# Performance work log

Hardware: AMD Instinct MI355X
Metric: run time of the kernel (lower is better)

## Reference

```python
import jax, jax.numpy as jnp
import numpy as np

B, C, N, H = 4, 256, 4096, 4
DK = C // H


def _proj(x, w, b):
    # Conv1d with kernel size 1 == per-point linear: [B,C,N] x [O,C] -> [B,O,N]
    return jnp.einsum('oc,bcn->bon', w, x) + b[None, :, None]


def setup_inputs() -> dict:
    key = jax.random.key(0)
    ks = jax.random.split(key, 9)
    s = 1.0 / np.sqrt(C)
    return {
        'x': jax.random.normal(ks[0], (B, C, N), jnp.float32),
        'wq': jax.random.normal(ks[1], (C, C), jnp.float32) * s,
        'bq': jax.random.normal(ks[2], (C,), jnp.float32) * 0.01,
        'wk': jax.random.normal(ks[3], (C, C), jnp.float32) * s,
        'bk': jax.random.normal(ks[4], (C,), jnp.float32) * 0.01,
        'wv': jax.random.normal(ks[5], (C, C), jnp.float32) * s,
        'bv': jax.random.normal(ks[6], (C,), jnp.float32) * 0.01,
        'wp': jax.random.normal(ks[7], (C, C), jnp.float32) * s,
        'bp': jax.random.normal(ks[8], (C,), jnp.float32) * 0.01,
    }


def reference(x, wq, bq, wk, bk, wv, bv, wp, bp):
    b, c, n = x.shape
    q = _proj(x, wq, bq).reshape(b, H, DK, n)
    k = _proj(x, wk, bk).reshape(b, H, DK, n)
    v = _proj(x, wv, bv).reshape(b, H, DK, n)
    scale = 1.0 / jnp.sqrt(jnp.asarray(DK, x.dtype))
    # scores over point pairs: [B,H,N,N]
    scores = jnp.einsum('bhdn,bhdm->bhnm', q, k) * scale
    attn = jax.nn.softmax(scores, axis=-1)
    out = jnp.einsum('bhnm,bhdm->bhdn', attn, v)  # [B,H,DK,N]
    out = out.reshape(b, c, n)
    out = _proj(out, wp, bp)
    return out + x
```

## Files before the change

### kernel.cpp

```cpp
#include <hip/hip_runtime.h>


#define BDIM 4
#define CDIM 256
#define NDIM 4096
#define HDIM 4
#define DKDIM 64
#define NQ   (BDIM * HDIM * NDIM)
#define QSCALE 0.18033688011112042f

typedef __bf16 bf16x8 __attribute__((ext_vector_type(8)));
typedef float f32x4 __attribute__((ext_vector_type(4)));
typedef short s16x4 __attribute__((ext_vector_type(4)));
typedef unsigned short u16;

__device__ __forceinline__ u16 f2bf(float f) {
  union { __bf16 h; u16 s; } u; u.h = (__bf16)f; return u.s;
}
__device__ __forceinline__ float bf2f(u16 v) {
  union { unsigned u; float f; } x; x.u = (unsigned)v << 16; return x.f;
}

__global__ __launch_bounds__(256) void wcvt_kernel(
    const float* __restrict__ w0, const float* __restrict__ w1,
    const float* __restrict__ w2, const float* __restrict__ w3,
    u16* __restrict__ d0, u16* __restrict__ d1,
    u16* __restrict__ d2, u16* __restrict__ d3)
{
  const int row = blockIdx.x;
  const int m = blockIdx.y;
  const float* s = (m == 0) ? w0 : (m == 1) ? w1 : (m == 2) ? w2 : w3;
  u16* d = (m == 0) ? d0 : (m == 1) ? d1 : (m == 2) ? d2 : d3;
  const float sc = (m == 0) ? QSCALE : 1.0f;
  const int idx = row * CDIM + threadIdx.x;
  d[idx] = f2bf(s[idx] * sc);
}

__global__ __launch_bounds__(256) void xt_kernel(
    const float* __restrict__ x, u16* __restrict__ xT)
{
  const int b = blockIdx.z, c0 = blockIdx.y * 64, n0 = blockIdx.x * 64;
  __shared__ __align__(16) float T[64][68];
  const int t = threadIdx.x;
  {
    const int cr = t >> 4, nc = (t & 15) * 4;
    #pragma unroll
    for (int ci = 0; ci < 4; ++ci) {
      const float4 v = *(const float4*)&x[((size_t)(b * CDIM + c0 + cr + ci * 16)) * NDIM + n0 + nc];
      *(float4*)&T[cr + ci * 16][nc] = v;
    }
  }
  __syncthreads();
  {
    const int n = t >> 2, g = t & 3;
    union { u16 u[16]; uint4 v[2]; } pk;
    #pragma unroll
    for (int u_ = 0; u_ < 16; ++u_) pk.u[u_] = f2bf(T[g * 16 + u_][n]);
    uint4* dst = (uint4*)&xT[((size_t)(b * NDIM + n0 + n)) * CDIM + c0 + g * 16];
    dst[0] = pk.v[0]; dst[1] = pk.v[1];
  }
}

template<int MODE>
__global__ __launch_bounds__(256, 4) void proj_kernel(
    const u16* __restrict__ xT, const u16* __restrict__ wb,
    const float* __restrict__ bias, const float* __restrict__ res,
    void* __restrict__ outp, float bscale)
{
  const int b = blockIdx.z, o0 = blockIdx.y * 64, n0 = blockIdx.x * 64;
  __shared__ __align__(16) u16 XTs[64][40];
  __shared__ __align__(16) u16 Ws[64][40];
  const int t = threadIdx.x, lane = t & 63, w = t >> 6;
  const int qd = lane >> 4, lm = lane & 15;
  const int sr = t >> 2, sg = (t & 3) * 8;

  const u16* xsrc = xT + ((size_t)(b * NDIM + n0 + sr)) * CDIM + sg;
  const u16* wsrc = wb + ((size_t)(o0 + sr)) * CDIM + sg;

  f32x4 acc[4];
  #pragma unroll
  for (int nt = 0; nt < 4; ++nt) acc[nt] = (f32x4){0.f, 0.f, 0.f, 0.f};

  for (int cs = 0; cs < 8; ++cs) {
    __syncthreads();
    *(uint4*)&XTs[sr][sg] = *(const uint4*)(xsrc + cs * 32);
    *(uint4*)&Ws[sr][sg]  = *(const uint4*)(wsrc + cs * 32);
    __syncthreads();
    bf16x8 xf[4];
    #pragma unroll
    for (int nt = 0; nt < 4; ++nt) xf[nt] = *(const bf16x8*)&XTs[16 * nt + lm][qd * 8];
    const bf16x8 wf = *(const bf16x8*)&Ws[16 * w + lm][qd * 8];
    #pragma unroll
    for (int nt = 0; nt < 4; ++nt) {
      if constexpr (MODE == 0)
        acc[nt] = __builtin_amdgcn_mfma_f32_16x16x32_bf16(xf[nt], wf, acc[nt], 0, 0, 0);
      else
        acc[nt] = __builtin_amdgcn_mfma_f32_16x16x32_bf16(wf, xf[nt], acc[nt], 0, 0, 0);
    }
  }

  if constexpr (MODE == 0) {
    u16* out = (u16*)outp;
    const int og = o0 + 16 * w + lm;
    const float bv = bias[og] * bscale;
    #pragma unroll
    for (int nt = 0; nt < 4; ++nt)
      #pragma unroll
      for (int r = 0; r < 4; ++r) {
        const int n = n0 + 16 * nt + 4 * qd + r;
        out[((size_t)(b * NDIM + n)) * CDIM + og] = f2bf(acc[nt][r] + bv);
      }
  } else {
    const float4 b4 = *(const float4*)&bias[o0 + 16 * w + 4 * qd];
    const float bvr[4] = {b4.x, b4.y, b4.z, b4.w};
    #pragma unroll
    for (int nt = 0; nt < 4; ++nt)
      #pragma unroll
      for (int r = 0; r < 4; ++r) {
        const int og = o0 + 16 * w + 4 * qd + r;
        const int n = n0 + 16 * nt + lm;
        const size_t idx = ((size_t)(b * CDIM + og)) * NDIM + n;
        const float val = acc[nt][r] + bvr[r];
        if constexpr (MODE == 1) ((u16*)outp)[idx] = f2bf(val);
        else ((float*)outp)[idx] = val + res[idx];
      }
  }
}

__global__ __launch_bounds__(256, 4) void attn_kernel(
    const u16* __restrict__ qT, const u16* __restrict__ kT,
    const u16* __restrict__ vB, u16* __restrict__ Opart,
    float* __restrict__ Mp, float* __restrict__ Lp)
{
  const int bh = blockIdx.y, b = bh >> 2, h = bh & 3;
  const int n0 = blockIdx.x * 128;
  const int z  = blockIdx.z;
  __shared__ __align__(16) u16 Qt[128][72];
  __shared__ __align__(16) u16 Kt[64][72];
  __shared__ __align__(16) u16 Vt[64][72];

  const int t = threadIdx.x, lane = t & 63, w = t >> 6;
  const int qd = lane >> 4, lm = lane & 15;

  {
    const int r = t >> 1, g = (t & 1) * 32;
    const uint4* src = (const uint4*)&qT[((size_t)(b * NDIM + n0 + r)) * CDIM + h * 64 + g];
    uint4* dst = (uint4*)&Qt[r][g];
    dst[0] = src[0]; dst[1] = src[1]; dst[2] = src[2]; dst[3] = src[3];
  }
  __syncthreads();
  bf16x8 qf[2][2];
  #pragma unroll
  for (int s = 0; s < 2; ++s)
    #pragma unroll
    for (int hh = 0; hh < 2; ++hh)
      qf[s][hh] = *(const bf16x8*)&Qt[16 * (2 * w + s) + lm][32 * hh + qd * 8];

  float m_i[2] = {-1e30f, -1e30f}, l_i[2] = {0.f, 0.f};
  f32x4 oa[2][4];
  #pragma unroll
  for (int s = 0; s < 2; ++s)
    #pragma unroll
    for (int dt = 0; dt < 4; ++dt) oa[s][dt] = (f32x4){0.f, 0.f, 0.f, 0.f};

  const int sr = t >> 2, sg = (t & 3) * 16;
  const u16* kptr = kT + ((size_t)(b * NDIM) + z * 2048 + sr) * CDIM + h * 64 + sg;
  const u16* vptr = vB + ((size_t)(b * CDIM) + h * 64 + sr) * NDIM + z * 2048 + sg;

  for (int it = 0; it < 32; ++it) {
    __syncthreads();
    {
      uint4* kd = (uint4*)&Kt[sr][sg];
      kd[0] = *(const uint4*)(kptr);
      kd[1] = *(const uint4*)(kptr + 8);
      uint4* vd = (uint4*)&Vt[sr][sg];
      vd[0] = *(const uint4*)(vptr);
      vd[1] = *(const uint4*)(vptr + 8);
    }
    kptr += (size_t)64 * CDIM;
    vptr += 64;
    __syncthreads();

    bf16x8 kf[4][2];
    #pragma unroll
    for (int nt = 0; nt < 4; ++nt)
      #pragma unroll
      for (int hh = 0; hh < 2; ++hh)
        kf[nt][hh] = *(const bf16x8*)&Kt[16 * nt + lm][32 * hh + qd * 8];

    float pr[2][4][4];
    #pragma unroll
    for (int s = 0; s < 2; ++s) {
      f32x4 sc[4];
      #pragma unroll
      for (int nt = 0; nt < 4; ++nt) {
        f32x4 zz = (f32x4){0.f, 0.f, 0.f, 0.f};
        zz = __builtin_amdgcn_mfma_f32_16x16x32_bf16(kf[nt][0], qf[s][0], zz, 0, 0, 0);
        zz = __builtin_amdgcn_mfma_f32_16x16x32_bf16(kf[nt][1], qf[s][1], zz, 0, 0, 0);
        sc[nt] = zz;
      }
      float mx = sc[0][0];
      #pragma unroll
      for (int nt = 0; nt < 4; ++nt)
        #pragma unroll
        for (int r = 0; r < 4; ++r) mx = fmaxf(mx, sc[nt][r]);
      mx = fmaxf(mx, __shfl_xor(mx, 16));
      mx = fmaxf(mx, __shfl_xor(mx, 32));
      const float mn = fmaxf(m_i[s], mx);
      if (__any(mx > m_i[s])) {
        const float al = __builtin_amdgcn_exp2f(m_i[s] - mn);
        l_i[s] *= al;
        #pragma unroll
        for (int dt = 0; dt < 4; ++dt) oa[s][dt] *= al;
      }
      m_i[s] = mn;
      float rs = 0.f;
      #pragma unroll
      for (int nt = 0; nt < 4; ++nt)
        #pragma unroll
        for (int r = 0; r < 4; ++r) {
          const float p = __builtin_amdgcn_exp2f(sc[nt][r] - mn);
          pr[s][nt][r] = p;
          rs += p;
        }
      rs += __shfl_xor(rs, 16);
      rs += __shfl_xor(rs, 32);
      l_i[s] += rs;
    }

    #pragma unroll
    for (int c = 0; c < 4; ++c) {
      s16x4 av[4];
      #pragma unroll
      for (int dt = 0; dt < 4; ++dt)
        av[dt] = *(const s16x4*)&Vt[16 * dt + lm][16 * c + 4 * qd];
      union { u16 u[4]; s16x4 v; } bp0, bp1;
      #pragma unroll
      for (int r = 0; r < 4; ++r) { bp0.u[r] = f2bf(pr[0][c][r]); bp1.u[r] = f2bf(pr[1][c][r]); }
      #pragma unroll
      for (int dt = 0; dt < 4; ++dt) {
        oa[0][dt] = __builtin_amdgcn_mfma_f32_16x16x16bf16_1k(av[dt], bp0.v, oa[0][dt], 0, 0, 0);
        oa[1][dt] = __builtin_amdgcn_mfma_f32_16x16x16bf16_1k(av[dt], bp1.v, oa[1][dt], 0, 0, 0);
      }
    }
  }

  __syncthreads();
  u16 (*Ot)[72] = (u16(*)[72])&Qt[0][0];
  #pragma unroll
  for (int s = 0; s < 2; ++s) {
    const float inv = 1.0f / l_i[s];
    #pragma unroll
    for (int dt = 0; dt < 4; ++dt)
      #pragma unroll
      for (int r = 0; r < 4; ++r)
        Ot[16 * (2 * w + s) + lm][16 * dt + 4 * qd + r] = f2bf(oa[s][dt][r] * inv);
  }
  if (qd == 0) {
    const size_t mlbase = ((size_t)z * (BDIM * HDIM) + bh) * NDIM;
    #pragma unroll
    for (int s = 0; s < 2; ++s) {
      const int q = n0 + 16 * (2 * w + s) + lm;
      Mp[mlbase + q] = m_i[s];
      Lp[mlbase + q] = l_i[s];
    }
  }
  __syncthreads();
  {
    const int r = t >> 1, g = (t & 1) * 32;
    u16* dst = Opart + (((size_t)z * (BDIM * HDIM) + bh) * NDIM + n0 + r) * DKDIM + g;
    const uint4* srcp = (const uint4*)&Ot[r][g];
    uint4* d4 = (uint4*)dst;
    d4[0] = srcp[0]; d4[1] = srcp[1]; d4[2] = srcp[2]; d4[3] = srcp[3];
  }
}

__global__ __launch_bounds__(256) void combine_kernel(
    const u16* __restrict__ Opart, const float* __restrict__ Mp,
    const float* __restrict__ Lp, u16* __restrict__ abT)
{
  const int t = threadIdx.x;
  const int gq = blockIdx.x * 64 + (t >> 2);
  const int seg = (t & 3) * 16;
  const float m0 = Mp[gq], l0 = Lp[gq];
  const float m1 = Mp[NQ + gq], l1 = Lp[NQ + gq];
  const float M = fmaxf(m0, m1);
  const float d0 = l0 * __builtin_amdgcn_exp2f(m0 - M);
  const float d1 = l1 * __builtin_amdgcn_exp2f(m1 - M);
  const float inv = 1.0f / (d0 + d1);
  const float w0 = d0 * inv, w1 = d1 * inv;

  const u16* p0 = Opart + (size_t)gq * DKDIM + seg;
  const u16* p1 = Opart + (size_t)NQ * DKDIM + (size_t)gq * DKDIM + seg;
  union { u16 u[16]; uint4 v[2]; } a0, a1, ov;
  a0.v[0] = ((const uint4*)p0)[0]; a0.v[1] = ((const uint4*)p0)[1];
  a1.v[0] = ((const uint4*)p1)[0]; a1.v[1] = ((const uint4*)p1)[1];
  #pragma unroll
  for (int j = 0; j < 16; ++j)
    ov.u[j] = f2bf(w0 * bf2f(a0.u[j]) + w1 * bf2f(a1.u[j]));

  const int bh = gq >> 12, n = gq & (NDIM - 1);
  const int b = bh >> 2, h = bh & 3;
  uint4* dst = (uint4*)&abT[((size_t)(b * NDIM + n)) * CDIM + h * 64 + seg];
  dst[0] = ov.v[0]; dst[1] = ov.v[1];
}

extern "C" void kernel_launch(void* const* d_in, const int* in_sizes, int n_in,
                              void* d_out, int out_size, void* d_ws, size_t ws_size,
                              hipStream_t stream)
{
  const float* x  = (const float*)d_in[0];
  const float* wq = (const float*)d_in[1];
  const float* bq = (const float*)d_in[2];
  const float* wk = (const float*)d_in[3];
  const float* bk = (const float*)d_in[4];
  const float* wv = (const float*)d_in[5];
  const float* bv = (const float*)d_in[6];
  const float* wp = (const float*)d_in[7];
  const float* bp = (const float*)d_in[8];
  float* out = (float*)d_out;

  const size_t sz  = (size_t)BDIM * CDIM * NDIM;
  const size_t wsz = (size_t)CDIM * CDIM;
  u16* xTb = (u16*)d_ws;
  u16* wqb = xTb + sz;
  u16* wkb = wqb + wsz;
  u16* wvb = wkb + wsz;
  u16* wpb = wvb + wsz;
  u16* qTb = wpb + wsz;
  u16* kTb = qTb + sz;
  u16* vBb = kTb + sz;
  u16* abT = vBb + sz;
  u16* Opart = abT + sz;
  float* Mp = (float*)(Opart + 2 * sz);
  float* Lp = Mp + 2 * (size_t)NQ;

  const dim3 blk(256);
  wcvt_kernel<<<dim3(CDIM, 4), blk, 0, stream>>>(wq, wk, wv, wp, wqb, wkb, wvb, wpb);
  xt_kernel<<<dim3(NDIM / 64, CDIM / 64, BDIM), blk, 0, stream>>>(x, xTb);
  const dim3 gp(NDIM / 64, 4, BDIM);
  proj_kernel<0><<<gp, blk, 0, stream>>>(xTb, wqb, bq, nullptr, qTb, QSCALE);
  proj_kernel<0><<<gp, blk, 0, stream>>>(xTb, wkb, bk, nullptr, kTb, 1.0f);
  proj_kernel<1><<<gp, blk, 0, stream>>>(xTb, wvb, bv, nullptr, vBb, 1.0f);
  attn_kernel<<<dim3(NDIM / 128, BDIM * HDIM, 2), blk, 0, stream>>>(qTb, kTb, vBb, Opart, Mp, Lp);
  combine_kernel<<<dim3(NQ / 64), blk, 0, stream>>>(Opart, Mp, Lp, abT);
  proj_kernel<2><<<gp, blk, 0, stream>>>(abT, wpb, bp, x, out, 1.0f);
}
```

Baseline: 232.0 us.

## Fuse weight conversion, QKV projections, and split-K combine into fewer kernels

Drops the separate weight-conversion kernel and converts fp32 weights to bf16 inside the projection tiles. The three Q/K/V projection launches become one launch with a grid dimension selecting the projection. The combine kernel is folded into the output projection, which merges the two attention partials on the fly while staging its input tile. This cuts launches and the abT round trip through memory, at the cost of redoing weight conversion in every tile and making the projection-select branch runtime rather than compile-time.

```diff
diff --git a/kernel.cpp b/kernel.cpp
--- a/kernel.cpp
+++ b/kernel.cpp
@@ -13,27 +13,16 @@
 typedef float f32x4 __attribute__((ext_vector_type(4)));
 typedef short s16x4 __attribute__((ext_vector_type(4)));
 typedef unsigned short u16;
+typedef unsigned int u32;
 
 __device__ __forceinline__ u16 f2bf(float f) {
   union { __bf16 h; u16 s; } u; u.h = (__bf16)f; return u.s;
 }
 __device__ __forceinline__ float bf2f(u16 v) {
-  union { unsigned u; float f; } x; x.u = (unsigned)v << 16; return x.f;
-}
-
-__global__ __launch_bounds__(256) void wcvt_kernel(
-    const float* __restrict__ w0, const float* __restrict__ w1,
-    const float* __restrict__ w2, const float* __restrict__ w3,
-    u16* __restrict__ d0, u16* __restrict__ d1,
-    u16* __restrict__ d2, u16* __restrict__ d3)
-{
-  const int row = blockIdx.x;
-  const int m = blockIdx.y;
-  const float* s = (m == 0) ? w0 : (m == 1) ? w1 : (m == 2) ? w2 : w3;
-  u16* d = (m == 0) ? d0 : (m == 1) ? d1 : (m == 2) ? d2 : d3;
-  const float sc = (m == 0) ? QSCALE : 1.0f;
-  const int idx = row * CDIM + threadIdx.x;
-  d[idx] = f2bf(s[idx] * sc);
+  union { u32 u; float f; } x; x.u = (u32)v << 16; return x.f;
+}
+__device__ __forceinline__ u32 pk2(float a, float b) {
+  return (u32)f2bf(a) | ((u32)f2bf(b) << 16);
 }
 
 __global__ __launch_bounds__(256) void xt_kernel(
@@ -61,13 +50,21 @@
   }
 }
 
-template<int MODE>
-__global__ __launch_bounds__(256, 4) void proj_kernel(
-    const u16* __restrict__ xT, const u16* __restrict__ wb,
-    const float* __restrict__ bias, const float* __restrict__ res,
-    void* __restrict__ outp, float bscale)
-{
-  const int b = blockIdx.z, o0 = blockIdx.y * 64, n0 = blockIdx.x * 64;
+__global__ __launch_bounds__(256, 4) void qkv_kernel(
+    const u16* __restrict__ xT,
+    const float* __restrict__ wq, const float* __restrict__ bq,
+    const float* __restrict__ wk, const float* __restrict__ bk,
+    const float* __restrict__ wv, const float* __restrict__ bv,
+    u16* __restrict__ qT, u16* __restrict__ kT, u16* __restrict__ vB)
+{
+  const int b = blockIdx.z;
+  const int p = blockIdx.y >> 2;
+  const int o0 = (blockIdx.y & 3) * 64;
+  const int n0 = blockIdx.x * 64;
+  const float* wsel = (p == 0) ? wq : (p == 1) ? wk : wv;
+  const float* bsel = (p == 0) ? bq : (p == 1) ? bk : bv;
+  const float wscale = (p == 0) ? QSCALE : 1.0f;
+
   __shared__ __align__(16) u16 XTs[64][40];
   __shared__ __align__(16) u16 Ws[64][40];
   const int t = threadIdx.x, lane = t & 63, w = t >> 6;
@@ -75,7 +72,7 @@
   const int sr = t >> 2, sg = (t & 3) * 8;
 
   const u16* xsrc = xT + ((size_t)(b * NDIM + n0 + sr)) * CDIM + sg;
-  const u16* wsrc = wb + ((size_t)(o0 + sr)) * CDIM + sg;
+  const float* wsrc = wsel + (size_t)(o0 + sr) * CDIM + sg;
 
   f32x4 acc[4];
   #pragma unroll
@@ -84,7 +81,16 @@
   for (int cs = 0; cs < 8; ++cs) {
     __syncthreads();
     *(uint4*)&XTs[sr][sg] = *(const uint4*)(xsrc + cs * 32);
-    *(uint4*)&Ws[sr][sg]  = *(const uint4*)(wsrc + cs * 32);
+    {
+      const float4 w0 = *(const float4*)(wsrc + cs * 32);
+      const float4 w1 = *(const float4*)(wsrc + cs * 32 + 4);
+      union { u32 p[4]; uint4 v; } pw;
+      pw.p[0] = pk2(w0.x * wscale, w0.y * wscale);
+      pw.p[1] = pk2(w0.z * wscale, w0.w * wscale);
+      pw.p[2] = pk2(w1.x * wscale, w1.y * wscale);
+      pw.p[3] = pk2(w1.z * wscale, w1.w * wscale);
+      *(uint4*)&Ws[sr][sg] = pw.v;
+    }
     __syncthreads();
     bf16x8 xf[4];
     #pragma unroll
@@ -92,26 +98,26 @@
     const bf16x8 wf = *(const bf16x8*)&Ws[16 * w + lm][qd * 8];
     #pragma unroll
     for (int nt = 0; nt < 4; ++nt) {
-      if constexpr (MODE == 0)
+      if (p < 2)
         acc[nt] = __builtin_amdgcn_mfma_f32_16x16x32_bf16(xf[nt], wf, acc[nt], 0, 0, 0);
       else
         acc[nt] = __builtin_amdgcn_mfma_f32_16x16x32_bf16(wf, xf[nt], acc[nt], 0, 0, 0);
     }
   }
 
-  if constexpr (MODE == 0) {
-    u16* out = (u16*)outp;
+  if (p < 2) {
+    u16* out = (p == 0) ? qT : kT;
     const int og = o0 + 16 * w + lm;
-    const float bv = bias[og] * bscale;
+    const float bv2 = bsel[og] * wscale;
     #pragma unroll
     for (int nt = 0; nt < 4; ++nt)
       #pragma unroll
       for (int r = 0; r < 4; ++r) {
         const int n = n0 + 16 * nt + 4 * qd + r;
-        out[((size_t)(b * NDIM + n)) * CDIM + og] = f2bf(acc[nt][r] + bv);
+        out[((size_t)(b * NDIM + n)) * CDIM + og] = f2bf(acc[nt][r] + bv2);
       }
   } else {
-    const float4 b4 = *(const float4*)&bias[o0 + 16 * w + 4 * qd];
+    const float4 b4 = *(const float4*)&bsel[o0 + 16 * w + 4 * qd];
     const float bvr[4] = {b4.x, b4.y, b4.z, b4.w};
     #pragma unroll
     for (int nt = 0; nt < 4; ++nt)
@@ -119,10 +125,7 @@
       for (int r = 0; r < 4; ++r) {
         const int og = o0 + 16 * w + 4 * qd + r;
         const int n = n0 + 16 * nt + lm;
-        const size_t idx = ((size_t)(b * CDIM + og)) * NDIM + n;
-        const float val = acc[nt][r] + bvr[r];
-        if constexpr (MODE == 1) ((u16*)outp)[idx] = f2bf(val);
-        else ((float*)outp)[idx] = val + res[idx];
+        vB[((size_t)(b * CDIM + og)) * NDIM + n] = f2bf(acc[nt][r] + bvr[r]);
       }
   }
 }
@@ -275,34 +278,83 @@
   }
 }
 
-__global__ __launch_bounds__(256) void combine_kernel(
+__global__ __launch_bounds__(256, 4) void projout_kernel(
     const u16* __restrict__ Opart, const float* __restrict__ Mp,
-    const float* __restrict__ Lp, u16* __restrict__ abT)
-{
-  const int t = threadIdx.x;
-  const int gq = blockIdx.x * 64 + (t >> 2);
-  const int seg = (t & 3) * 16;
-  const float m0 = Mp[gq], l0 = Lp[gq];
-  const float m1 = Mp[NQ + gq], l1 = Lp[NQ + gq];
-  const float M = fmaxf(m0, m1);
-  const float d0 = l0 * __builtin_amdgcn_exp2f(m0 - M);
-  const float d1 = l1 * __builtin_amdgcn_exp2f(m1 - M);
-  const float inv = 1.0f / (d0 + d1);
-  const float w0 = d0 * inv, w1 = d1 * inv;
-
-  const u16* p0 = Opart + (size_t)gq * DKDIM + seg;
-  const u16* p1 = Opart + (size_t)NQ * DKDIM + (size_t)gq * DKDIM + seg;
-  union { u16 u[16]; uint4 v[2]; } a0, a1, ov;
-  a0.v[0] = ((const uint4*)p0)[0]; a0.v[1] = ((const uint4*)p0)[1];
-  a1.v[0] = ((const uint4*)p1)[0]; a1.v[1] = ((const uint4*)p1)[1];
-  #pragma unroll
-  for (int j = 0; j < 16; ++j)
-    ov.u[j] = f2bf(w0 * bf2f(a0.u[j]) + w1 * bf2f(a1.u[j]));
-
-  const int bh = gq >> 12, n = gq & (NDIM - 1);
-  const int b = bh >> 2, h = bh & 3;
-  uint4* dst = (uint4*)&abT[((size_t)(b * NDIM + n)) * CDIM + h * 64 + seg];
-  dst[0] = ov.v[0]; dst[1] = ov.v[1];
+    const float* __restrict__ Lp, const float* __restrict__ wp,
+    const float* __restrict__ bp, const float* __restrict__ res,
+    float* __restrict__ out)
+{
+  const int b = blockIdx.z, o0 = blockIdx.y * 64, n0 = blockIdx.x * 64;
+  __shared__ __align__(16) u16 XTs[64][40];
+  __shared__ __align__(16) u16 Ws[64][40];
+  const int t = threadIdx.x, lane = t & 63, w = t >> 6;
+  const int qd = lane >> 4, lm = lane & 15;
+  const int sr = t >> 2, sg = (t & 3) * 8;
+
+  float w0h[4], w1h[4];
+  #pragma unroll
+  for (int hh = 0; hh < 4; ++hh) {
+    const size_t i0 = ((size_t)(b * HDIM + hh)) * NDIM + n0 + sr;
+    const size_t i1 = (size_t)NQ + i0;
+    const float m0 = Mp[i0], l0 = Lp[i0];
+    const float m1 = Mp[i1], l1 = Lp[i1];
+    const float M = fmaxf(m0, m1);
+    const float d0 = l0 * __builtin_amdgcn_exp2f(m0 - M);
+    const float d1 = l1 * __builtin_amdgcn_exp2f(m1 - M);
+    const float iv = 1.0f / (d0 + d1);
+    w0h[hh] = d0 * iv; w1h[hh] = d1 * iv;
+  }
+
+  const float* wsrc = wp + (size_t)(o0 + sr) * CDIM + sg;
+
+  f32x4 acc[4];
+  #pragma unroll
+  for (int nt = 0; nt < 4; ++nt) acc[nt] = (f32x4){0.f, 0.f, 0.f, 0.f};
+
+  for (int cs = 0; cs < 8; ++cs) {
+    const int c0 = cs * 32;
+    const int hh = c0 >> 6;
+    const int dk = (c0 & 63) + sg;
+    __syncthreads();
+    {
+      const size_t obase = (((size_t)(b * HDIM + hh)) * NDIM + n0 + sr) * DKDIM + dk;
+      union { u16 u[8]; uint4 v; } a0, a1, ov;
+      a0.v = *(const uint4*)(Opart + obase);
+      a1.v = *(const uint4*)(Opart + (size_t)NQ * DKDIM + obase);
+      #pragma unroll
+      for (int j = 0; j < 8; ++j)
+        ov.u[j] = f2bf(w0h[hh] * bf2f(a0.u[j]) + w1h[hh] * bf2f(a1.u[j]));
+      *(uint4*)&XTs[sr][sg] = ov.v;
+      const float4 wv0 = *(const float4*)(wsrc + c0);
+      const float4 wv1 = *(const float4*)(wsrc + c0 + 4);
+      union { u32 p[4]; uint4 v; } pw;
+      pw.p[0] = pk2(wv0.x, wv0.y);
+      pw.p[1] = pk2(wv0.z, wv0.w);
+      pw.p[2] = pk2(wv1.x, wv1.y);
+      pw.p[3] = pk2(wv1.z, wv1.w);
+      *(uint4*)&Ws[sr][sg] = pw.v;
+    }
+    __syncthreads();
+    bf16x8 xf[4];
+    #pragma unroll
+    for (int nt = 0; nt < 4; ++nt) xf[nt] = *(const bf16x8*)&XTs[16 * nt + lm][qd * 8];
+    const bf16x8 wf = *(const bf16x8*)&Ws[16 * w + lm][qd * 8];
+    #pragma unroll
+    for (int nt = 0; nt < 4; ++nt)
+      acc[nt] = __builtin_amdgcn_mfma_f32_16x16x32_bf16(wf, xf[nt], acc[nt], 0, 0, 0);
+  }
+
+  const float4 b4 = *(const float4*)&bp[o0 + 16 * w + 4 * qd];
+  const float bvr[4] = {b4.x, b4.y, b4.z, b4.w};
+  #pragma unroll
+  for (int nt = 0; nt < 4; ++nt)
+    #pragma unroll
+    for (int r = 0; r < 4; ++r) {
+      const int og = o0 + 16 * w + 4 * qd + r;
+      const int n = n0 + 16 * nt + lm;
+      const size_t idx = ((size_t)(b * CDIM + og)) * NDIM + n;
+      out[idx] = acc[nt][r] + bvr[r] + res[idx];
+    }
 }
 
 extern "C" void kernel_launch(void* const* d_in, const int* in_sizes, int n_in,
@@ -320,29 +372,21 @@
   const float* bp = (const float*)d_in[8];
   float* out = (float*)d_out;
 
-  const size_t sz  = (size_t)BDIM * CDIM * NDIM;
-  const size_t wsz = (size_t)CDIM * CDIM;
+  const size_t sz = (size_t)BDIM * CDIM * NDIM;
   u16* xTb = (u16*)d_ws;
-  u16* wqb = xTb + sz;
-  u16* wkb = wqb + wsz;
-  u16* wvb = wkb + wsz;
-  u16* wpb = wvb + wsz;
-  u16* qTb = wpb + wsz;
+  u16* qTb = xTb + sz;
   u16* kTb = qTb + sz;
   u16* vBb = kTb + sz;
-  u16* abT = vBb + sz;
-  u16* Opart = abT + sz;
+  u16* Opart = vBb + sz;
   float* Mp = (float*)(Opart + 2 * sz);
   float* Lp = Mp + 2 * (size_t)NQ;
 
   const dim3 blk(256);
-  wcvt_kernel<<<dim3(CDIM, 4), blk, 0, stream>>>(wq, wk, wv, wp, wqb, wkb, wvb, wpb);
   xt_kernel<<<dim3(NDIM / 64, CDIM / 64, BDIM), blk, 0, stream>>>(x, xTb);
-  const dim3 gp(NDIM / 64, 4, BDIM);
-  proj_kernel<0><<<gp, blk, 0, stream>>>(xTb, wqb, bq, nullptr, qTb, QSCALE);
-  proj_kernel<0><<<gp, blk, 0, stream>>>(xTb, wkb, bk, nullptr, kTb, 1.0f);
-  proj_kernel<1><<<gp, blk, 0, stream>>>(xTb, wvb, bv, nullptr, vBb, 1.0f);
-  attn_kernel<<<dim3(NDIM / 128, BDIM * HDIM, 2), blk, 0, stream>>>(qTb, kTb, vBb, Opart, Mp, Lp);
-  combine_kernel<<<dim3(NQ / 64), blk, 0, stream>>>(Opart, Mp, Lp, abT);
-  proj_kernel<2><<<gp, blk, 0, stream>>>(abT, wpb, bp, x, out, 1.0f);
-}
+  qkv_kernel<<<dim3(NDIM / 64, 12, BDIM), blk, 0, stream>>>(
+      xTb, wq, bq, wk, bk, wv, bv, qTb, kTb, vBb);
+  attn_kernel<<<dim3(NDIM / 128, BDIM * HDIM, 2), blk, 0, stream>>>(
+      qTb, kTb, vBb, Opart, Mp, Lp);
+  projout_kernel<<<dim3(NDIM / 64, 4, BDIM), blk, 0, stream>>>(
+      Opart, Mp, Lp, wp, bp, x, out);
+}
```

After: 217.7 us. 1.07x faster.
